# Kernel tuning notes

Hardware: AMD Instinct MI355X
Metric: run time of the kernel (lower is better)

## Reference

```python
import jax, jax.numpy as jnp
from jax import lax
import numpy as np

EPS_LN = 1e-5
EPS_BN = 1e-5


def _forward(x, prior, alpha, in_proj_w, conv_w, conv_b, x_proj_weight,
             dt_projs_weight, dt_projs_bias, A_logs, Ds, out_norm_w, out_norm_b,
             out_proj_w, p2w_w1, p2w_b1, p2w_bn_w, p2w_bn_b, p2w_bn_mean,
             p2w_bn_var, p2w_w2, p2w_b2):
    Din = conv_w.shape[0]
    # in_proj (Linear2d == 1x1 conv), split into ssm branch and gate z
    xz = jnp.einsum('bchw,dc->bdhw', x, in_proj_w)          # [B, 2*Din, H, W]
    x_ssm, z = jnp.split(xz, 2, axis=1)
    # depthwise 3x3 conv + SiLU
    x_ssm = lax.conv_general_dilated(
        x_ssm, conv_w, (1, 1), 'SAME',
        dimension_numbers=('NCHW', 'OIHW', 'NCHW'),
        feature_group_count=Din) + conv_b[None, :, None, None]
    x_ssm = jax.nn.silu(x_ssm)

    B, D, H, W = x_ssm.shape
    L = H * W
    K = 4
    R = dt_projs_weight.shape[2]
    N = A_logs.shape[1]

    # cross_scan: 4 directions = row-major, col-major, and their reverses
    row = x_ssm.reshape(B, D, L)
    col = x_ssm.transpose(0, 1, 3, 2).reshape(B, D, L)
    xs = jnp.stack([row, col, row[..., ::-1], col[..., ::-1]], axis=1)  # [B,K,D,L]

    x_dbl = jnp.einsum('bkdl,kcd->bkcl', xs, x_proj_weight)  # [B,K,R+2N,L]
    dts, Bs, Cs = jnp.split(x_dbl, [R, R + N], axis=2)       # [B,K,R,L],[B,K,N,L],[B,K,N,L]
    dts = jnp.einsum('bkrl,kdr->bkdl', dts, dt_projs_weight)  # [B,K,D,L]

    A = -jnp.exp(A_logs.astype(jnp.float32)).reshape(K, D, N)
    dt = jax.nn.softplus(dts + dt_projs_bias[None, :, :, None])  # [B,K,D,L]

    dA = jnp.exp(dt[..., None] * A[None, :, :, None, :])          # [B,K,D,L,N]
    dBx = dt[..., None] * Bs.transpose(0, 1, 3, 2)[:, :, None, :, :] * xs[..., None]
    Cseq = Cs.transpose(0, 1, 3, 2)                               # [B,K,L,N]

    dA_t = jnp.moveaxis(dA, 3, 0)    # [L,B,K,D,N]
    dBx_t = jnp.moveaxis(dBx, 3, 0)  # [L,B,K,D,N]
    C_t = jnp.moveaxis(Cseq, 2, 0)   # [L,B,K,N]

    def step(h, inp):
        a, bx, c = inp
        h = h * a + bx                              # [B,K,D,N]
        y = jnp.einsum('bkdn,bkn->bkd', h, c)
        return h, y

    h0 = jnp.zeros((B, K, D, N), dtype=jnp.float32)
    _, ys = lax.scan(step, h0, (dA_t, dBx_t, C_t))  # [L,B,K,D]
    ys = jnp.moveaxis(ys, 0, 3)                     # [B,K,D,L]
    ys = ys + Ds.reshape(K, D)[None, :, :, None] * xs
    ys = ys.reshape(B, K, D, H, W)

    # prior -> per-direction guidance weights (PriorToWeights, BN in eval mode)
    g = jnp.einsum('bchw,oc->bohw', prior, p2w_w1) + p2w_b1[None, :, None, None]
    g = (g - p2w_bn_mean[None, :, None, None]) * jax.lax.rsqrt(
        p2w_bn_var[None, :, None, None] + EPS_BN)
    g = g * p2w_bn_w[None, :, None, None] + p2w_bn_b[None, :, None, None]
    g = jax.nn.relu(g)
    g = jnp.einsum('bchw,oc->bohw', g, p2w_w2) + p2w_b2[None, :, None, None]
    gw = jax.nn.sigmoid(g)                          # [B,4,H,W]
    s = jax.nn.sigmoid(alpha)                       # [1]
    Wdir = 1.0 + s * (gw - 1.0)                     # torch.lerp(ones, gw, s)
    ys = ys * Wdir[:, :, None, :, :]

    # cross_merge: inverse of cross_scan, sum of 4 directions
    ysl = ys.reshape(B, K, D, L)
    y = ysl[:, 0] + ysl[:, 2, :, ::-1]
    yt = ysl[:, 1] + ysl[:, 3, :, ::-1]
    y = y + yt.reshape(B, D, W, H).transpose(0, 1, 3, 2).reshape(B, D, L)
    y = y.reshape(B, D, H, W)

    # LayerNorm2d: normalize over channel dim
    mu = y.mean(axis=1, keepdims=True)
    var = y.var(axis=1, keepdims=True)
    y = (y - mu) * jax.lax.rsqrt(var + EPS_LN)
    y = y * out_norm_w[None, :, None, None] + out_norm_b[None, :, None, None]

    y = y * jax.nn.silu(z)
    out = jnp.einsum('bdhw,md->bmhw', y, out_proj_w)  # out_proj 1x1, no bias
    return out


def setup_inputs() -> dict:
    key = jax.random.key(0)
    ks = jax.random.split(key, 16)
    B, Dm, H, W = 8, 96, 64, 64
    Din, N, K, R, hid = 192, 1, 4, 6, 32

    def rn(k, shape, scale):
        return jax.random.normal(k, shape, jnp.float32) * scale

    return {
        'x': rn(ks[0], (B, Dm, H, W), 1.0),
        'prior': jax.random.uniform(ks[1], (B, 4, H, W), jnp.float32),
        'alpha': rn(ks[2], (1,), 1.0),
        'in_proj_w': rn(ks[3], (2 * Din, Dm), Dm ** -0.5),
        'conv_w': rn(ks[4], (Din, 1, 3, 3), 1.0 / 3.0),
        'conv_b': rn(ks[5], (Din,), 0.1),
        'x_proj_weight': rn(ks[6], (K, R + 2 * N, Din), Din ** -0.5),
        'dt_projs_weight': rn(ks[7], (K, Din, R), R ** -0.5),
        'dt_projs_bias': rn(ks[8], (K, Din), 0.5) - 4.0,
        'A_logs': jnp.tile(jnp.log(jnp.arange(1, N + 1, dtype=jnp.float32)), (K * Din, 1)),
        'Ds': jnp.ones((K * Din,), jnp.float32),
        'out_norm_w': jnp.ones((Din,), jnp.float32),
        'out_norm_b': jnp.zeros((Din,), jnp.float32),
        'out_proj_w': rn(ks[9], (Dm, Din), Din ** -0.5),
        'p2w_w1': rn(ks[10], (hid, 4), 0.5),
        'p2w_b1': jnp.zeros((hid,), jnp.float32),
        'p2w_bn_w': jnp.ones((hid,), jnp.float32),
        'p2w_bn_b': jnp.zeros((hid,), jnp.float32),
        'p2w_bn_mean': jnp.zeros((hid,), jnp.float32),
        'p2w_bn_var': jnp.ones((hid,), jnp.float32),
        'p2w_w2': rn(ks[11], (4, hid), hid ** -0.5),
        'p2w_b2': jnp.zeros((4,), jnp.float32),
    }


def reference(x, prior, alpha, in_proj_w, conv_w, conv_b, x_proj_weight,
              dt_projs_weight, dt_projs_bias, A_logs, Ds, out_norm_w, out_norm_b,
              out_proj_w, p2w_w1, p2w_b1, p2w_bn_w, p2w_bn_b, p2w_bn_mean,
              p2w_bn_var, p2w_w2, p2w_b2):
    return _forward(x, prior, alpha, in_proj_w, conv_w, conv_b, x_proj_weight,
                    dt_projs_weight, dt_projs_bias, A_logs, Ds, out_norm_w,
                    out_norm_b, out_proj_w, p2w_w1, p2w_b1, p2w_bn_w, p2w_bn_b,
                    p2w_bn_mean, p2w_bn_var, p2w_w2, p2w_b2)
```

## Files before the change

### kernel.cpp

```cpp
#include <hip/hip_runtime.h>

#define BB   8
#define CIN  96
#define DIN  192
#define HH   64
#define WW   64
#define LL   4096
#define KK   4
#define COUT 96
#define SS   128
#define LC   32

#define LOG2E 1.4426950408889634f
#define LN2   0.6931471805599453f

__device__ __forceinline__ float exp2fast(float x) { return __builtin_amdgcn_exp2f(x); }
__device__ __forceinline__ float log2fast(float x) { return __builtin_amdgcn_logf(x); }
__device__ __forceinline__ float sigf(float x) { return 1.0f / (1.0f + __expf(-x)); }
__device__ __forceinline__ int trp(int p) { return ((p & 63) << 6) | (p >> 6); }
__device__ __forceinline__ int pix_of(int k, int l) {
  if (k == 0) return l;
  if (k == 1) return trp(l);
  if (k == 2) return LL - 1 - l;
  return trp(LL - 1 - l);
}

template <int C, int OT>
__global__ __launch_bounds__(256) void gemm_pix_k(const float* __restrict__ in,
                                                  const float* __restrict__ W,
                                                  float* __restrict__ out, int O) {
  const int tid = threadIdx.x;
  const int b  = blockIdx.z;
  const int o0 = blockIdx.y * OT;
  const int p0 = blockIdx.x * 1024 + tid * 4;
  const float* inb = in + (size_t)b * C * LL + p0;
  const float* Wb  = W + (size_t)o0 * C;
  float4 acc[OT];
#pragma unroll
  for (int j = 0; j < OT; ++j) acc[j] = make_float4(0.f, 0.f, 0.f, 0.f);
#pragma unroll 4
  for (int c = 0; c < C; c += 4) {
    float4 w[OT];
#pragma unroll
    for (int j = 0; j < OT; ++j) w[j] = *(const float4*)&Wb[j * C + c];
    float4 xv[4];
#pragma unroll
    for (int t = 0; t < 4; ++t) xv[t] = *(const float4*)&inb[(size_t)(c + t) * LL];
#pragma unroll
    for (int j = 0; j < OT; ++j) {
#pragma unroll
      for (int t = 0; t < 4; ++t) {
        const float ws = t == 0 ? w[j].x : t == 1 ? w[j].y : t == 2 ? w[j].z : w[j].w;
        acc[j].x = fmaf(xv[t].x, ws, acc[j].x);
        acc[j].y = fmaf(xv[t].y, ws, acc[j].y);
        acc[j].z = fmaf(xv[t].z, ws, acc[j].z);
        acc[j].w = fmaf(xv[t].w, ws, acc[j].w);
      }
    }
  }
  float* ob = out + (size_t)b * O * LL + p0;
#pragma unroll
  for (int j = 0; j < OT; ++j) *(float4*)&ob[(size_t)(o0 + j) * LL] = acc[j];
}

__global__ __launch_bounds__(256) void p2w_k(const float* __restrict__ prior,
                                             const float* __restrict__ alpha,
                                             const float* __restrict__ w1,
                                             const float* __restrict__ b1,
                                             const float* __restrict__ bnw,
                                             const float* __restrict__ bnb,
                                             const float* __restrict__ bnm,
                                             const float* __restrict__ bnv,
                                             const float* __restrict__ w2,
                                             const float* __restrict__ b2,
                                             const float* __restrict__ xpw,
                                             float* __restrict__ xpwT,
                                             float* __restrict__ Wg) {
  if (blockIdx.x == 0) {
    for (int idx = threadIdx.x; idx < KK * DIN * 8; idx += 256) {
      int kk = idx / (DIN * 8);
      int rem = idx % (DIN * 8);
      int dd = rem >> 3, c = rem & 7;
      xpwT[idx] = xpw[(kk * 8 + c) * DIN + dd];
    }
  }
  int idx = blockIdx.x * 256 + threadIdx.x;
  int p = idx & (LL - 1);
  int b = idx >> 12;
  float pr[4];
#pragma unroll
  for (int c = 0; c < 4; ++c) pr[c] = prior[((size_t)b * 4 + c) * LL + p];
  float s = sigf(alpha[0]);
  float g2[4];
#pragma unroll
  for (int j = 0; j < 4; ++j) g2[j] = b2[j];
  for (int o = 0; o < 32; ++o) {
    float g = b1[o];
#pragma unroll
    for (int c = 0; c < 4; ++c) g = fmaf(pr[c], w1[o * 4 + c], g);
    g = (g - bnm[o]) * rsqrtf(bnv[o] + 1e-5f) * bnw[o] + bnb[o];
    g = fmaxf(g, 0.0f);
#pragma unroll
    for (int j = 0; j < 4; ++j) g2[j] = fmaf(g, w2[j * 32 + o], g2[j]);
  }
#pragma unroll
  for (int j = 0; j < 4; ++j)
    Wg[((size_t)b * 4 + j) * LL + p] = 1.0f + s * (sigf(g2[j]) - 1.0f);
}

__global__ __launch_bounds__(1024) void convproj_k(const float* __restrict__ xz,
                                                   const float* __restrict__ cw,
                                                   const float* __restrict__ cb,
                                                   const float* __restrict__ xpwT,
                                                   float* __restrict__ xcT,
                                                   float* __restrict__ projS) {
  __shared__ float sX[96 * 65];
  __shared__ float4 sP[512];
  const int tid = threadIdx.x;
  const int b = blockIdx.y;
  const int h = blockIdx.x;
  const int px = tid & 63;
  const int ku = __builtin_amdgcn_readfirstlane((tid >> 6) & 3);
  const int hf = __builtin_amdgcn_readfirstlane((tid >> 8) & 1);
  const int q  = __builtin_amdgcn_readfirstlane(tid >> 9);
  float a0 = 0.0f, a1 = 0.0f, a2 = 0.0f, a3 = 0.0f;

#pragma unroll
  for (int half = 0; half < 2; ++half) {
    for (int idx = tid; idx < 96 * 16; idx += 1024) {
      int ddl = idx >> 4, pq = idx & 15;
      int w0 = pq * 4;
      int dd = half * 96 + ddl;
      const float* base = xz + ((size_t)b * 384 + dd) * LL + h * 64 + w0;
      const float* wp = cw + dd * 9;
      float bv = cb[dd];
      float s0 = bv, s1 = bv, s2 = bv, s3 = bv;
#pragma unroll
      for (int dh = -1; dh <= 1; ++dh) {
        int hh = h + dh;
        if (hh < 0 || hh >= HH) continue;
        const float* row = base + dh * 64;
        float4 cm = *(const float4*)row;
        float lf = (w0 > 0)  ? row[-1] : 0.0f;
        float rt = (w0 < 60) ? row[4]  : 0.0f;
        float c0 = wp[(dh + 1) * 3], c1 = wp[(dh + 1) * 3 + 1], c2 = wp[(dh + 1) * 3 + 2];
        s0 = fmaf(lf,   c0, s0); s0 = fmaf(cm.x, c1, s0); s0 = fmaf(cm.y, c2, s0);
        s1 = fmaf(cm.x, c0, s1); s1 = fmaf(cm.y, c1, s1); s1 = fmaf(cm.z, c2, s1);
        s2 = fmaf(cm.y, c0, s2); s2 = fmaf(cm.z, c1, s2); s2 = fmaf(cm.w, c2, s2);
        s3 = fmaf(cm.z, c0, s3); s3 = fmaf(cm.w, c1, s3); s3 = fmaf(rt,   c2, s3);
      }
      float* so = &sX[ddl * 65 + w0];
      so[0] = s0 * sigf(s0);
      so[1] = s1 * sigf(s1);
      so[2] = s2 * sigf(s2);
      so[3] = s3 * sigf(s3);
    }
    __syncthreads();
    for (int idx = tid; idx < 64 * 96; idx += 1024) {
      int pp = idx / 96, ddl = idx % 96;
      xcT[((size_t)b * LL + h * 64 + pp) * DIN + half * 96 + ddl] = sX[ddl * 65 + pp];
    }
    {
      const int ddl0 = q * 48;
      const float* wp = xpwT + (size_t)ku * (DIN * 8) + (half * 96 + ddl0) * 8 + hf * 4;
#pragma unroll 8
      for (int d48 = 0; d48 < 48; ++d48) {
        float xv = sX[(ddl0 + d48) * 65 + px];
        const float4 w4 = *(const float4*)(wp + d48 * 8);
        a0 = fmaf(xv, w4.x, a0);
        a1 = fmaf(xv, w4.y, a1);
        a2 = fmaf(xv, w4.z, a2);
        a3 = fmaf(xv, w4.w, a3);
      }
    }
    __syncthreads();
  }
  const int slot = tid & 511;
  if (q == 1) sP[slot] = make_float4(a0, a1, a2, a3);
  __syncthreads();
  if (q == 0) {
    float4 o = sP[slot];
    a0 += o.x; a1 += o.y; a2 += o.z; a3 += o.w;
    const int p = h * 64 + px;
    int l;
    if (ku == 0) l = p;
    else if (ku == 1) l = trp(p);
    else if (ku == 2) l = LL - 1 - p;
    else l = LL - 1 - trp(p);
    float* pb = projS + (((size_t)b * KK + ku) * LL + l) * 8 + hf * 4;
    *(float4*)pb = make_float4(a0, a1, a2, a3);
  }
}

__global__ __launch_bounds__(192) void scan_part_k(const float* __restrict__ xcT,
                                                   const float* __restrict__ projS,
                                                   const float* __restrict__ dtw,
                                                   const float* __restrict__ dtb,
                                                   const float* __restrict__ A_logs,
                                                   float* __restrict__ carrP,
                                                   float* __restrict__ carrH) {
  const int s = blockIdx.x, kp = blockIdx.y, b = blockIdx.z;
  const int d = threadIdx.x;
  const int kA = kp, kB = kp + 2;
  const int s2 = SS - 1 - s;
  const int kdA = kA * DIN + d, kdB = kB * DIN + d;
  float wrA[6], wrB[6];
#pragma unroll
  for (int r = 0; r < 6; ++r) { wrA[r] = dtw[kdA * 6 + r]; wrB[r] = dtw[kdB * 6 + r]; }
  const float biasA = dtb[kdA], biasB = dtb[kdB];
  const float AaA = -__expf(A_logs[kdA]), AaB = -__expf(A_logs[kdB]);
  const int l0 = s * LC;
  const int p0 = pix_of(kA, l0);
  const int dp = pix_of(kA, l0 + 1) - p0;
  const float* xp = xcT + ((size_t)b * LL + p0) * DIN + d;
  const long xstep = (long)dp * DIN;
  const float* prA = projS + (((size_t)b * KK + kA) * LL + l0) * 8;
  const float* prB = projS + (((size_t)b * KK + kB) * LL + s2 * LC + (LC - 1)) * 8;
  float PA = 1.0f, HA = 0.0f, PB = 1.0f, HB = 0.0f;
#pragma unroll 2
  for (int j = 0; j < LC; ++j) {
    float4 a0 = *(const float4*)prA;
    float4 a1 = *(const float4*)(prA + 4);
    prA += 8;
    float4 b0 = *(const float4*)prB;
    float4 b1 = *(const float4*)(prB + 4);
    prB -= 8;
    float xv = *xp;
    xp += xstep;
    {
      float dtr = biasA;
      dtr = fmaf(a0.x, wrA[0], dtr);
      dtr = fmaf(a0.y, wrA[1], dtr);
      dtr = fmaf(a0.z, wrA[2], dtr);
      dtr = fmaf(a0.w, wrA[3], dtr);
      dtr = fmaf(a1.x, wrA[4], dtr);
      dtr = fmaf(a1.y, wrA[5], dtr);
      float e = exp2fast(fminf(dtr, 80.0f) * LOG2E);
      float u = log2fast(1.0f + e);
      float a = exp2fast(u * AaA);
      float dt = u * LN2;
      HA = fmaf(a, HA, dt * a1.z * xv);
      PA *= a;
    }
    {
      float dtr = biasB;
      dtr = fmaf(b0.x, wrB[0], dtr);
      dtr = fmaf(b0.y, wrB[1], dtr);
      dtr = fmaf(b0.z, wrB[2], dtr);
      dtr = fmaf(b0.w, wrB[3], dtr);
      dtr = fmaf(b1.x, wrB[4], dtr);
      dtr = fmaf(b1.y, wrB[5], dtr);
      float e = exp2fast(fminf(dtr, 80.0f) * LOG2E);
      float u = log2fast(1.0f + e);
      float a = exp2fast(u * AaB);
      float dt = u * LN2;
      HB = fmaf(PB, dt * b1.z * xv, HB);
      PB *= a;
    }
  }
  size_t oA = ((size_t)((b * KK + kA) * SS + s)) * DIN + d;
  size_t oB = ((size_t)((b * KK + kB) * SS + s2)) * DIN + d;
  carrP[oA] = PA;
  carrH[oA] = HA;
  carrP[oB] = PB;
  carrH[oB] = HB;
}

__global__ __launch_bounds__(192) void scan_fix_k(const float* __restrict__ carrP,
                                                  const float* __restrict__ carrH,
                                                  float* __restrict__ h0) {
  const int k = blockIdx.x, b = blockIdx.y, d = threadIdx.x;
  size_t base = ((size_t)(b * KK + k)) * SS * DIN + d;
  float h = 0.0f;
#pragma unroll 4
  for (int s = 0; s < SS; ++s) {
    h0[base + (size_t)s * DIN] = h;
    h = fmaf(carrP[base + (size_t)s * DIN], h, carrH[base + (size_t)s * DIN]);
  }
}

__global__ __launch_bounds__(192) void scan_apply_k(const float* __restrict__ xcT,
                                                    const float* __restrict__ projS,
                                                    const float* __restrict__ Wg,
                                                    const float* __restrict__ h0,
                                                    const float* __restrict__ dtw,
                                                    const float* __restrict__ dtb,
                                                    const float* __restrict__ A_logs,
                                                    const float* __restrict__ Ds,
                                                    float* __restrict__ ymT,
                                                    float* __restrict__ ymT2) {
  const int s = blockIdx.x, kp = blockIdx.y, b = blockIdx.z;
  const int d = threadIdx.x;
  __shared__ float sAcc[LC * DIN];
  float xr[LC];
  {
    const int k = kp, kd = k * DIN + d;
    float wr[6];
#pragma unroll
    for (int r = 0; r < 6; ++r) wr[r] = dtw[kd * 6 + r];
    const float bias = dtb[kd];
    const float Aa = -__expf(A_logs[kd]);
    const float Dv = Ds[kd];
    const int l0 = s * LC;
    const int p0 = pix_of(k, l0);
    const int dp = pix_of(k, l0 + 1) - p0;
    const float* xp = xcT + ((size_t)b * LL + p0) * DIN + d;
    const long xstep = (long)dp * DIN;
    const float* pr = projS + (((size_t)b * KK + k) * LL + l0) * 8;
    const float* wg = Wg + ((size_t)b * KK + k) * LL + l0;
    float h = h0[((size_t)((b * KK + k) * SS + s)) * DIN + d];
#pragma unroll
    for (int j = 0; j < LC; ++j) {
      float4 q0 = *(const float4*)pr;
      float4 q1 = *(const float4*)(pr + 4);
      pr += 8;
      float xv = *xp;
      xp += xstep;
      xr[j] = xv;
      float dtr = bias;
      dtr = fmaf(q0.x, wr[0], dtr);
      dtr = fmaf(q0.y, wr[1], dtr);
      dtr = fmaf(q0.z, wr[2], dtr);
      dtr = fmaf(q0.w, wr[3], dtr);
      dtr = fmaf(q1.x, wr[4], dtr);
      dtr = fmaf(q1.y, wr[5], dtr);
      float e = exp2fast(fminf(dtr, 80.0f) * LOG2E);
      float u = log2fast(1.0f + e);
      float a = exp2fast(u * Aa);
      float dt = u * LN2;
      h = fmaf(a, h, dt * q1.z * xv);
      sAcc[j * DIN + d] = fmaf(h, q1.w, Dv * xv) * wg[j];
    }
  }
  {
    const int k = kp + 2, kd = k * DIN + d;
    const int s2 = SS - 1 - s;
    float wr[6];
#pragma unroll
    for (int r = 0; r < 6; ++r) wr[r] = dtw[kd * 6 + r];
    const float bias = dtb[kd];
    const float Aa = -__expf(A_logs[kd]);
    const float Dv = Ds[kd];
    const int l0 = s2 * LC;
    const float* pr = projS + (((size_t)b * KK + k) * LL + l0) * 8;
    const float* wg = Wg + ((size_t)b * KK + k) * LL + l0;
    float h = h0[((size_t)((b * KK + k) * SS + s2)) * DIN + d];
#pragma unroll
    for (int j = 0; j < LC; ++j) {
      float4 q0 = *(const float4*)pr;
      float4 q1 = *(const float4*)(pr + 4);
      pr += 8;
      float xv = xr[LC - 1 - j];
      float dtr = bias;
      dtr = fmaf(q0.x, wr[0], dtr);
      dtr = fmaf(q0.y, wr[1], dtr);
      dtr = fmaf(q0.z, wr[2], dtr);
      dtr = fmaf(q0.w, wr[3], dtr);
      dtr = fmaf(q1.x, wr[4], dtr);
      dtr = fmaf(q1.y, wr[5], dtr);
      float e = exp2fast(fminf(dtr, 80.0f) * LOG2E);
      float u = log2fast(1.0f + e);
      float a = exp2fast(u * Aa);
      float dt = u * LN2;
      h = fmaf(a, h, dt * q1.z * xv);
      float y = fmaf(h, q1.w, Dv * xv) * wg[j];
      sAcc[(LC - 1 - j) * DIN + d] += y;
    }
  }
  float* dst;
  if (kp == 0)
    dst = ymT + (size_t)b * (384 * (size_t)LL) + (size_t)(s * LC) * DIN + d;
  else
    dst = ymT2 + ((size_t)b * LL + s * LC) * DIN + d;
#pragma unroll 4
  for (int j = 0; j < LC; ++j) dst[(size_t)j * DIN] = sAcc[j * DIN + d];
}

__global__ __launch_bounds__(256) void ln_silu_k(const float* __restrict__ ymT,
                                                 const float* __restrict__ ymT2,
                                                 const float* __restrict__ xz,
                                                 const float* __restrict__ gamma,
                                                 const float* __restrict__ beta,
                                                 float* __restrict__ u) {
  const int b = blockIdx.y;
  const int h = blockIdx.x;
  const int p0 = h * 64;
  __shared__ float sY[64 * 193];
  __shared__ float sS[4][64], sQ[4][64];
  const int tid = threadIdx.x;
  const float* ymb = ymT + (size_t)b * (384 * (size_t)LL);
  for (int idx = tid; idx < 64 * DIN; idx += 256) {
    int pp = idx / DIN, dd = idx % DIN;
    float v = ymb[(size_t)(p0 + pp) * DIN + dd] +
              ymT2[((size_t)b * LL + pp * 64 + h) * DIN + dd];
    sY[pp * 193 + dd] = v;
  }
  __syncthreads();
  const int px = tid & 63, g = tid >> 6;
  float sum = 0.0f, ss = 0.0f;
  for (int dd = g * 48; dd < g * 48 + 48; ++dd) {
    float v = sY[px * 193 + dd];
    sum += v;
    ss = fmaf(v, v, ss);
  }
  sS[g][px] = sum;
  sQ[g][px] = ss;
  __syncthreads();
  sum = sS[0][px] + sS[1][px] + sS[2][px] + sS[3][px];
  ss  = sQ[0][px] + sQ[1][px] + sQ[2][px] + sQ[3][px];
  const float mu = sum * (1.0f / DIN);
  float var = ss * (1.0f / DIN) - mu * mu;
  const float rstd = rsqrtf(fmaxf(var, 0.0f) + 1e-5f);
  const float* zb = xz + ((size_t)b * 384 + DIN) * LL + p0 + px;
  float* ub = u + (size_t)b * DIN * LL + p0 + px;
  for (int dd = g * 48; dd < g * 48 + 48; ++dd) {
    float v = sY[px * 193 + dd];
    float z = zb[(size_t)dd * LL];
    float tn = fmaf((v - mu) * rstd, gamma[dd], beta[dd]);
    ub[(size_t)dd * LL] = tn * (z * sigf(z));
  }
}

extern "C" void kernel_launch(void* const* d_in, const int* in_sizes, int n_in,
                              void* d_out, int out_size, void* d_ws, size_t ws_size,
                              hipStream_t stream) {
  const float* x      = (const float*)d_in[0];
  const float* prior  = (const float*)d_in[1];
  const float* alpha  = (const float*)d_in[2];
  const float* ipw    = (const float*)d_in[3];
  const float* cw     = (const float*)d_in[4];
  const float* cb     = (const float*)d_in[5];
  const float* xpw    = (const float*)d_in[6];
  const float* dtw    = (const float*)d_in[7];
  const float* dtb    = (const float*)d_in[8];
  const float* A_logs = (const float*)d_in[9];
  const float* Ds     = (const float*)d_in[10];
  const float* onw    = (const float*)d_in[11];
  const float* onb    = (const float*)d_in[12];
  const float* opw    = (const float*)d_in[13];
  const float* w1     = (const float*)d_in[14];
  const float* b1     = (const float*)d_in[15];
  const float* bnw    = (const float*)d_in[16];
  const float* bnb    = (const float*)d_in[17];
  const float* bnm    = (const float*)d_in[18];
  const float* bnv    = (const float*)d_in[19];
  const float* w2     = (const float*)d_in[20];
  const float* b2     = (const float*)d_in[21];
  float* out = (float*)d_out;

  char* ws = (char*)d_ws;
  float* xz    = (float*)(ws);
  float* xcT   = (float*)(ws + 50331648);
  float* ymT2  = (float*)(ws + 75497472);
  float* projS = (float*)(ws + 100663296);
  float* Wgb   = (float*)(ws + 104857600);
  float* carrP = (float*)(ws + 105381888);
  float* carrH = (float*)(ws + 108527616);
  float* h0b   = (float*)(ws + 111673344);
  float* xpwT  = (float*)(ws + 114819072);
  float* ymT   = xz;
  float* u     = xcT;

  gemm_pix_k<CIN, 8><<<dim3(LL / 1024, 384 / 8, BB), 256, 0, stream>>>(x, ipw, xz, 384);
  p2w_k<<<(BB * LL) / 256, 256, 0, stream>>>(prior, alpha, w1, b1, bnw, bnb, bnm,
                                             bnv, w2, b2, xpw, xpwT, Wgb);
  convproj_k<<<dim3(HH, BB), 1024, 0, stream>>>(xz, cw, cb, xpwT, xcT, projS);
  scan_part_k<<<dim3(SS, 2, BB), 192, 0, stream>>>(xcT, projS, dtw, dtb, A_logs,
                                                   carrP, carrH);
  scan_fix_k<<<dim3(KK, BB), 192, 0, stream>>>(carrP, carrH, h0b);
  scan_apply_k<<<dim3(SS, 2, BB), 192, 0, stream>>>(xcT, projS, Wgb, h0b, dtw, dtb,
                                                    A_logs, Ds, ymT, ymT2);
  ln_silu_k<<<dim3(HH, BB), 256, 0, stream>>>(ymT, ymT2, xz, onw, onb, u);
  gemm_pix_k<DIN, 4><<<dim3(LL / 1024, COUT / 4, BB), 256, 0, stream>>>(u, opw, out, COUT);
}
```

Measured before the change: 187.0 us.

## Store intermediate activations in bf16 to halve global memory traffic

All large intermediate buffers (xz, xcT, ymT/ymT2, u) are now stored as bf16 with round-to-nearest-even conversion, and every kernel converts back to float at load time. This targets the memory-bandwidth cost of writing and reading these multi-megabyte tensors across the eight kernels. The workspace layout is compacted to match. It adds rounding error to the activations that the scan and layer norm consume, which could hurt accuracy against the fp32 reference. Scattered 2-byte stores such as the xcT transpose may coalesce less well.

```diff
diff --git a/kernel.cpp b/kernel.cpp
--- a/kernel.cpp
+++ b/kernel.cpp
@@ -14,6 +14,8 @@
 #define LOG2E 1.4426950408889634f
 #define LN2   0.6931471805599453f
 
+typedef unsigned short bf16t;
+
 __device__ __forceinline__ float exp2fast(float x) { return __builtin_amdgcn_exp2f(x); }
 __device__ __forceinline__ float log2fast(float x) { return __builtin_amdgcn_logf(x); }
 __device__ __forceinline__ float sigf(float x) { return 1.0f / (1.0f + __expf(-x)); }
@@ -24,30 +26,36 @@
   if (k == 2) return LL - 1 - l;
   return trp(LL - 1 - l);
 }
-
-template <int C, int OT>
-__global__ __launch_bounds__(256) void gemm_pix_k(const float* __restrict__ in,
-                                                  const float* __restrict__ W,
-                                                  float* __restrict__ out, int O) {
+__device__ __forceinline__ float b2f(bf16t v) {
+  return __uint_as_float((unsigned)v << 16);
+}
+__device__ __forceinline__ bf16t f2b(float f) {
+  unsigned u = __float_as_uint(f);
+  return (bf16t)((u + 0x7FFFu + ((u >> 16) & 1u)) >> 16);
+}
+
+__global__ __launch_bounds__(256) void gemm_in_k(const float* __restrict__ in,
+                                                 const float* __restrict__ W,
+                                                 bf16t* __restrict__ out) {
   const int tid = threadIdx.x;
   const int b  = blockIdx.z;
-  const int o0 = blockIdx.y * OT;
+  const int o0 = blockIdx.y * 8;
   const int p0 = blockIdx.x * 1024 + tid * 4;
-  const float* inb = in + (size_t)b * C * LL + p0;
-  const float* Wb  = W + (size_t)o0 * C;
-  float4 acc[OT];
-#pragma unroll
-  for (int j = 0; j < OT; ++j) acc[j] = make_float4(0.f, 0.f, 0.f, 0.f);
+  const float* inb = in + (size_t)b * CIN * LL + p0;
+  const float* Wb  = W + (size_t)o0 * CIN;
+  float4 acc[8];
+#pragma unroll
+  for (int j = 0; j < 8; ++j) acc[j] = make_float4(0.f, 0.f, 0.f, 0.f);
 #pragma unroll 4
-  for (int c = 0; c < C; c += 4) {
-    float4 w[OT];
-#pragma unroll
-    for (int j = 0; j < OT; ++j) w[j] = *(const float4*)&Wb[j * C + c];
+  for (int c = 0; c < CIN; c += 4) {
+    float4 w[8];
+#pragma unroll
+    for (int j = 0; j < 8; ++j) w[j] = *(const float4*)&Wb[j * CIN + c];
     float4 xv[4];
 #pragma unroll
     for (int t = 0; t < 4; ++t) xv[t] = *(const float4*)&inb[(size_t)(c + t) * LL];
 #pragma unroll
-    for (int j = 0; j < OT; ++j) {
+    for (int j = 0; j < 8; ++j) {
 #pragma unroll
       for (int t = 0; t < 4; ++t) {
         const float ws = t == 0 ? w[j].x : t == 1 ? w[j].y : t == 2 ? w[j].z : w[j].w;
@@ -58,9 +66,56 @@
       }
     }
   }
-  float* ob = out + (size_t)b * O * LL + p0;
-#pragma unroll
-  for (int j = 0; j < OT; ++j) *(float4*)&ob[(size_t)(o0 + j) * LL] = acc[j];
+  bf16t* ob = out + (size_t)b * 384 * LL + p0;
+#pragma unroll
+  for (int j = 0; j < 8; ++j) {
+    ushort4 st;
+    st.x = f2b(acc[j].x);
+    st.y = f2b(acc[j].y);
+    st.z = f2b(acc[j].z);
+    st.w = f2b(acc[j].w);
+    *(ushort4*)&ob[(size_t)(o0 + j) * LL] = st;
+  }
+}
+
+__global__ __launch_bounds__(256) void gemm_out_k(const bf16t* __restrict__ in,
+                                                  const float* __restrict__ W,
+                                                  float* __restrict__ out) {
+  const int tid = threadIdx.x;
+  const int b  = blockIdx.z;
+  const int o0 = blockIdx.y * 4;
+  const int p0 = blockIdx.x * 1024 + tid * 4;
+  const bf16t* inb = in + (size_t)b * DIN * LL + p0;
+  const float* Wb  = W + (size_t)o0 * DIN;
+  float4 acc[4];
+#pragma unroll
+  for (int j = 0; j < 4; ++j) acc[j] = make_float4(0.f, 0.f, 0.f, 0.f);
+#pragma unroll 4
+  for (int c = 0; c < DIN; c += 4) {
+    float4 w[4];
+#pragma unroll
+    for (int j = 0; j < 4; ++j) w[j] = *(const float4*)&Wb[j * DIN + c];
+    float4 xv[4];
+#pragma unroll
+    for (int t = 0; t < 4; ++t) {
+      ushort4 xu = *(const ushort4*)&inb[(size_t)(c + t) * LL];
+      xv[t] = make_float4(b2f(xu.x), b2f(xu.y), b2f(xu.z), b2f(xu.w));
+    }
+#pragma unroll
+    for (int j = 0; j < 4; ++j) {
+#pragma unroll
+      for (int t = 0; t < 4; ++t) {
+        const float ws = t == 0 ? w[j].x : t == 1 ? w[j].y : t == 2 ? w[j].z : w[j].w;
+        acc[j].x = fmaf(xv[t].x, ws, acc[j].x);
+        acc[j].y = fmaf(xv[t].y, ws, acc[j].y);
+        acc[j].z = fmaf(xv[t].z, ws, acc[j].z);
+        acc[j].w = fmaf(xv[t].w, ws, acc[j].w);
+      }
+    }
+  }
+  float* ob = out + (size_t)b * COUT * LL + p0;
+#pragma unroll
+  for (int j = 0; j < 4; ++j) *(float4*)&ob[(size_t)(o0 + j) * LL] = acc[j];
 }
 
 __global__ __launch_bounds__(256) void p2w_k(const float* __restrict__ prior,
@@ -108,11 +163,11 @@
     Wg[((size_t)b * 4 + j) * LL + p] = 1.0f + s * (sigf(g2[j]) - 1.0f);
 }
 
-__global__ __launch_bounds__(1024) void convproj_k(const float* __restrict__ xz,
+__global__ __launch_bounds__(1024) void convproj_k(const bf16t* __restrict__ xz,
                                                    const float* __restrict__ cw,
                                                    const float* __restrict__ cb,
                                                    const float* __restrict__ xpwT,
-                                                   float* __restrict__ xcT,
+                                                   bf16t* __restrict__ xcT,
                                                    float* __restrict__ projS) {
   __shared__ float sX[96 * 65];
   __shared__ float4 sP[512];
@@ -131,7 +186,7 @@
       int ddl = idx >> 4, pq = idx & 15;
       int w0 = pq * 4;
       int dd = half * 96 + ddl;
-      const float* base = xz + ((size_t)b * 384 + dd) * LL + h * 64 + w0;
+      const bf16t* base = xz + ((size_t)b * 384 + dd) * LL + h * 64 + w0;
       const float* wp = cw + dd * 9;
       float bv = cb[dd];
       float s0 = bv, s1 = bv, s2 = bv, s3 = bv;
@@ -139,15 +194,16 @@
       for (int dh = -1; dh <= 1; ++dh) {
         int hh = h + dh;
         if (hh < 0 || hh >= HH) continue;
-        const float* row = base + dh * 64;
-        float4 cm = *(const float4*)row;
-        float lf = (w0 > 0)  ? row[-1] : 0.0f;
-        float rt = (w0 < 60) ? row[4]  : 0.0f;
+        const bf16t* row = base + dh * 64;
+        ushort4 cmu = *(const ushort4*)row;
+        float cmx = b2f(cmu.x), cmy = b2f(cmu.y), cmz = b2f(cmu.z), cmw = b2f(cmu.w);
+        float lf = (w0 > 0)  ? b2f(row[-1]) : 0.0f;
+        float rt = (w0 < 60) ? b2f(row[4])  : 0.0f;
         float c0 = wp[(dh + 1) * 3], c1 = wp[(dh + 1) * 3 + 1], c2 = wp[(dh + 1) * 3 + 2];
-        s0 = fmaf(lf,   c0, s0); s0 = fmaf(cm.x, c1, s0); s0 = fmaf(cm.y, c2, s0);
-        s1 = fmaf(cm.x, c0, s1); s1 = fmaf(cm.y, c1, s1); s1 = fmaf(cm.z, c2, s1);
-        s2 = fmaf(cm.y, c0, s2); s2 = fmaf(cm.z, c1, s2); s2 = fmaf(cm.w, c2, s2);
-        s3 = fmaf(cm.z, c0, s3); s3 = fmaf(cm.w, c1, s3); s3 = fmaf(rt,   c2, s3);
+        s0 = fmaf(lf,  c0, s0); s0 = fmaf(cmx, c1, s0); s0 = fmaf(cmy, c2, s0);
+        s1 = fmaf(cmx, c0, s1); s1 = fmaf(cmy, c1, s1); s1 = fmaf(cmz, c2, s1);
+        s2 = fmaf(cmy, c0, s2); s2 = fmaf(cmz, c1, s2); s2 = fmaf(cmw, c2, s2);
+        s3 = fmaf(cmz, c0, s3); s3 = fmaf(cmw, c1, s3); s3 = fmaf(rt,  c2, s3);
       }
       float* so = &sX[ddl * 65 + w0];
       so[0] = s0 * sigf(s0);
@@ -158,7 +214,8 @@
     __syncthreads();
     for (int idx = tid; idx < 64 * 96; idx += 1024) {
       int pp = idx / 96, ddl = idx % 96;
-      xcT[((size_t)b * LL + h * 64 + pp) * DIN + half * 96 + ddl] = sX[ddl * 65 + pp];
+      xcT[((size_t)b * LL + h * 64 + pp) * DIN + half * 96 + ddl] =
+          f2b(sX[ddl * 65 + pp]);
     }
     {
       const int ddl0 = q * 48;
@@ -192,7 +249,7 @@
   }
 }
 
-__global__ __launch_bounds__(192) void scan_part_k(const float* __restrict__ xcT,
+__global__ __launch_bounds__(192) void scan_part_k(const bf16t* __restrict__ xcT,
                                                    const float* __restrict__ projS,
                                                    const float* __restrict__ dtw,
                                                    const float* __restrict__ dtb,
@@ -212,7 +269,7 @@
   const int l0 = s * LC;
   const int p0 = pix_of(kA, l0);
   const int dp = pix_of(kA, l0 + 1) - p0;
-  const float* xp = xcT + ((size_t)b * LL + p0) * DIN + d;
+  const bf16t* xp = xcT + ((size_t)b * LL + p0) * DIN + d;
   const long xstep = (long)dp * DIN;
   const float* prA = projS + (((size_t)b * KK + kA) * LL + l0) * 8;
   const float* prB = projS + (((size_t)b * KK + kB) * LL + s2 * LC + (LC - 1)) * 8;
@@ -225,7 +282,7 @@
     float4 b0 = *(const float4*)prB;
     float4 b1 = *(const float4*)(prB + 4);
     prB -= 8;
-    float xv = *xp;
+    float xv = b2f(*xp);
     xp += xstep;
     {
       float dtr = biasA;
@@ -279,7 +336,7 @@
   }
 }
 
-__global__ __launch_bounds__(192) void scan_apply_k(const float* __restrict__ xcT,
+__global__ __launch_bounds__(192) void scan_apply_k(const bf16t* __restrict__ xcT,
                                                     const float* __restrict__ projS,
                                                     const float* __restrict__ Wg,
                                                     const float* __restrict__ h0,
@@ -287,8 +344,8 @@
                                                     const float* __restrict__ dtb,
                                                     const float* __restrict__ A_logs,
                                                     const float* __restrict__ Ds,
-                                                    float* __restrict__ ymT,
-                                                    float* __restrict__ ymT2) {
+                                                    bf16t* __restrict__ ymT,
+                                                    bf16t* __restrict__ ymT2) {
   const int s = blockIdx.x, kp = blockIdx.y, b = blockIdx.z;
   const int d = threadIdx.x;
   __shared__ float sAcc[LC * DIN];
@@ -304,7 +361,7 @@
     const int l0 = s * LC;
     const int p0 = pix_of(k, l0);
     const int dp = pix_of(k, l0 + 1) - p0;
-    const float* xp = xcT + ((size_t)b * LL + p0) * DIN + d;
+    const bf16t* xp = xcT + ((size_t)b * LL + p0) * DIN + d;
     const long xstep = (long)dp * DIN;
     const float* pr = projS + (((size_t)b * KK + k) * LL + l0) * 8;
     const float* wg = Wg + ((size_t)b * KK + k) * LL + l0;
@@ -314,7 +371,7 @@
       float4 q0 = *(const float4*)pr;
       float4 q1 = *(const float4*)(pr + 4);
       pr += 8;
-      float xv = *xp;
+      float xv = b2f(*xp);
       xp += xstep;
       xr[j] = xv;
       float dtr = bias;
@@ -367,32 +424,32 @@
       sAcc[(LC - 1 - j) * DIN + d] += y;
     }
   }
-  float* dst;
+  bf16t* dst;
   if (kp == 0)
     dst = ymT + (size_t)b * (384 * (size_t)LL) + (size_t)(s * LC) * DIN + d;
   else
     dst = ymT2 + ((size_t)b * LL + s * LC) * DIN + d;
 #pragma unroll 4
-  for (int j = 0; j < LC; ++j) dst[(size_t)j * DIN] = sAcc[j * DIN + d];
-}
-
-__global__ __launch_bounds__(256) void ln_silu_k(const float* __restrict__ ymT,
-                                                 const float* __restrict__ ymT2,
-                                                 const float* __restrict__ xz,
+  for (int j = 0; j < LC; ++j) dst[(size_t)j * DIN] = f2b(sAcc[j * DIN + d]);
+}
+
+__global__ __launch_bounds__(256) void ln_silu_k(const bf16t* __restrict__ ymT,
+                                                 const bf16t* __restrict__ ymT2,
+                                                 const bf16t* __restrict__ xz,
                                                  const float* __restrict__ gamma,
                                                  const float* __restrict__ beta,
-                                                 float* __restrict__ u) {
+                                                 bf16t* __restrict__ u) {
   const int b = blockIdx.y;
   const int h = blockIdx.x;
   const int p0 = h * 64;
   __shared__ float sY[64 * 193];
   __shared__ float sS[4][64], sQ[4][64];
   const int tid = threadIdx.x;
-  const float* ymb = ymT + (size_t)b * (384 * (size_t)LL);
+  const bf16t* ymb = ymT + (size_t)b * (384 * (size_t)LL);
   for (int idx = tid; idx < 64 * DIN; idx += 256) {
     int pp = idx / DIN, dd = idx % DIN;
-    float v = ymb[(size_t)(p0 + pp) * DIN + dd] +
-              ymT2[((size_t)b * LL + pp * 64 + h) * DIN + dd];
+    float v = b2f(ymb[(size_t)(p0 + pp) * DIN + dd]) +
+              b2f(ymT2[((size_t)b * LL + pp * 64 + h) * DIN + dd]);
     sY[pp * 193 + dd] = v;
   }
   __syncthreads();
@@ -411,13 +468,13 @@
   const float mu = sum * (1.0f / DIN);
   float var = ss * (1.0f / DIN) - mu * mu;
   const float rstd = rsqrtf(fmaxf(var, 0.0f) + 1e-5f);
-  const float* zb = xz + ((size_t)b * 384 + DIN) * LL + p0 + px;
-  float* ub = u + (size_t)b * DIN * LL + p0 + px;
+  const bf16t* zb = xz + ((size_t)b * 384 + DIN) * LL + p0 + px;
+  bf16t* ub = u + (size_t)b * DIN * LL + p0 + px;
   for (int dd = g * 48; dd < g * 48 + 48; ++dd) {
     float v = sY[px * 193 + dd];
-    float z = zb[(size_t)dd * LL];
+    float z = b2f(zb[(size_t)dd * LL]);
     float tn = fmaf((v - mu) * rstd, gamma[dd], beta[dd]);
-    ub[(size_t)dd * LL] = tn * (z * sigf(z));
+    ub[(size_t)dd * LL] = f2b(tn * (z * sigf(z)));
   }
 }
 
@@ -449,19 +506,19 @@
   float* out = (float*)d_out;
 
   char* ws = (char*)d_ws;
-  float* xz    = (float*)(ws);
-  float* xcT   = (float*)(ws + 50331648);
-  float* ymT2  = (float*)(ws + 75497472);
-  float* projS = (float*)(ws + 100663296);
-  float* Wgb   = (float*)(ws + 104857600);
-  float* carrP = (float*)(ws + 105381888);
-  float* carrH = (float*)(ws + 108527616);
-  float* h0b   = (float*)(ws + 111673344);
-  float* xpwT  = (float*)(ws + 114819072);
-  float* ymT   = xz;
-  float* u     = xcT;
-
-  gemm_pix_k<CIN, 8><<<dim3(LL / 1024, 384 / 8, BB), 256, 0, stream>>>(x, ipw, xz, 384);
+  bf16t* xz    = (bf16t*)(ws);
+  bf16t* xcT   = (bf16t*)(ws + 25165824);
+  bf16t* ymT2  = (bf16t*)(ws + 37748736);
+  float* projS = (float*)(ws + 50331648);
+  float* Wgb   = (float*)(ws + 54525952);
+  float* carrP = (float*)(ws + 55050240);
+  float* carrH = (float*)(ws + 58195968);
+  float* h0b   = (float*)(ws + 61341696);
+  float* xpwT  = (float*)(ws + 64487424);
+  bf16t* ymT   = xz;
+  bf16t* u     = xcT;
+
+  gemm_in_k<<<dim3(LL / 1024, 384 / 8, BB), 256, 0, stream>>>(x, ipw, xz);
   p2w_k<<<(BB * LL) / 256, 256, 0, stream>>>(prior, alpha, w1, b1, bnw, bnb, bnm,
                                              bnv, w2, b2, xpw, xpwT, Wgb);
   convproj_k<<<dim3(HH, BB), 1024, 0, stream>>>(xz, cw, cb, xpwT, xcT, projS);
@@ -471,5 +528,5 @@
   scan_apply_k<<<dim3(SS, 2, BB), 192, 0, stream>>>(xcT, projS, Wgb, h0b, dtw, dtb,
                                                     A_logs, Ds, ymT, ymT2);
   ln_silu_k<<<dim3(HH, BB), 256, 0, stream>>>(ymT, ymT2, xz, onw, onb, u);
-  gemm_pix_k<DIN, 4><<<dim3(LL / 1024, COUT / 4, BB), 256, 0, stream>>>(u, opw, out, COUT);
-}
+  gemm_out_k<<<dim3(LL / 1024, COUT / 4, BB), 256, 0, stream>>>(u, opw, out);
+}
```

Measured after the change: 182.8 us. 2.2% less time.
